# Kernel optimization log

Measured on AMD Instinct MI355X. Metric: run time of the kernel, lower is better.

## Reference

```python
import jax, jax.numpy as jnp
import numpy as np

NUM_NODES = 100000
NUM_EDGES = 625000
IN_FEATURES = 128
OUT_FEATURES = 128


def setup_inputs() -> dict:
    key = jax.random.key(0)
    k1, k2, k3, k4 = jax.random.split(key, 4)
    x = jax.random.normal(k1, (NUM_NODES, IN_FEATURES), dtype=jnp.float32)
    edge_index = jax.random.randint(k2, (2, NUM_EDGES), 0, NUM_NODES, dtype=jnp.int64)
    # Xavier uniform for W (fan_in=IN, fan_out=OUT); B initialized to zeros in the
    # original, but we use small random values so gradients flow through both paths.
    limit = float(np.sqrt(6.0 / (IN_FEATURES + OUT_FEATURES)))
    W = jax.random.uniform(k3, (OUT_FEATURES, IN_FEATURES), dtype=jnp.float32,
                           minval=-limit, maxval=limit)
    B = jax.random.uniform(k4, (OUT_FEATURES, IN_FEATURES), dtype=jnp.float32,
                           minval=-limit, maxval=limit)
    return {"x": x, "edge_index": edge_index, "W": W, "B": B}


def reference(x, edge_index, W, B):
    sources, destinations = edge_index[0], edge_index[1]
    # message: gather destination features, scatter-add into source slots
    messages = x[destinations]                                        # [E, F_in]
    agg = jax.ops.segment_sum(messages, sources, num_segments=x.shape[0])  # [N, F_in]
    # in-degree (w.r.t. sources) normalization; zero-degree -> divide by 1
    deg = jax.ops.segment_sum(jnp.ones((sources.shape[0],), dtype=x.dtype),
                              sources, num_segments=x.shape[0])       # [N]
    deg = jnp.where(deg == 0, jnp.ones_like(deg), deg)
    agg = agg / deg[:, None]
    # update: (W @ messages.T + B @ x.T).T == messages @ W.T + x @ B.T
    out = agg @ W.T + x @ B.T                                         # [N, F_out]
    return out
```

## Files before the change

kernel.cpp:

```cpp
#include <hip/hip_runtime.h>

#define F_IN   128
#define F_OUT  128

typedef __attribute__((ext_vector_type(8))) short short8;
typedef __attribute__((ext_vector_type(4))) float floatx4;

__device__ __forceinline__ float bf16u_to_f_lo(unsigned int u) {
    union { unsigned int i; float f; } c; c.i = u << 16; return c.f;
}
__device__ __forceinline__ float bf16u_to_f_hi(unsigned int u) {
    union { unsigned int i; float f; } c; c.i = u & 0xffff0000u; return c.f;
}
__device__ __forceinline__ unsigned short f_to_bf16(float f) {
    union { float f; unsigned int i; } c; c.f = f;
    unsigned int u = c.i;
    u += 0x7fffu + ((u >> 16) & 1u);
    return (unsigned short)(u >> 16);
}
__device__ __forceinline__ unsigned int pack2(unsigned short a, unsigned short b) {
    return (unsigned int)a | ((unsigned int)b << 16);
}

__global__ void zero_kernel(int* __restrict__ p, long n) {
    long i = (long)blockIdx.x * blockDim.x + threadIdx.x;
    long stride = (long)gridDim.x * blockDim.x;
    for (; i < n; i += stride) p[i] = 0;
}

__global__ void hist_kernel(const int* __restrict__ src, int* __restrict__ cnt, int E) {
    int e = blockIdx.x * blockDim.x + threadIdx.x;
    if (e < E) atomicAdd(&cnt[src[e]], 1);
}

__global__ __launch_bounds__(256) void chunk_sums_kernel(const int* __restrict__ cnt,
                                                         int* __restrict__ partials, int n) {
    __shared__ int s[256];
    int b = blockIdx.x, t = threadIdx.x;
    int base = b * 1024 + t * 4;
    int sum = 0;
#pragma unroll
    for (int j = 0; j < 4; ++j) {
        int i = base + j;
        if (i < n) sum += cnt[i];
    }
    s[t] = sum;
    __syncthreads();
    for (int d = 128; d > 0; d >>= 1) {
        if (t < d) s[t] += s[t + d];
        __syncthreads();
    }
    if (t == 0) partials[b] = s[0];
}

__global__ __launch_bounds__(128) void scan_partials_kernel(const int* __restrict__ partials,
                                                            int* __restrict__ chunk_off, int nch) {
    __shared__ int s[128];
    int t = threadIdx.x;
    s[t] = (t < nch) ? partials[t] : 0;
    __syncthreads();
    for (int d = 1; d < 128; d <<= 1) {
        int val = s[t];
        int add = (t >= d) ? s[t - d] : 0;
        __syncthreads();
        s[t] = val + add;
        __syncthreads();
    }
    if (t < nch) chunk_off[t] = (t > 0) ? s[t - 1] : 0;
}

__global__ __launch_bounds__(256) void scan_chunks_kernel(int* __restrict__ off,
                                                          const int* __restrict__ chunk_off,
                                                          int n) {
    __shared__ int s[256];
    int b = blockIdx.x, t = threadIdx.x;
    int base = b * 1024 + t * 4;
    int v[4];
#pragma unroll
    for (int j = 0; j < 4; ++j) {
        int i = base + j;
        v[j] = (i < n) ? off[i] : 0;
    }
    int l1 = v[0], l2 = l1 + v[1], l3 = l2 + v[2], tot = l3 + v[3];
    s[t] = tot;
    __syncthreads();
    for (int d = 1; d < 256; d <<= 1) {
        int val = s[t];
        int add = (t >= d) ? s[t - d] : 0;
        __syncthreads();
        s[t] = val + add;
        __syncthreads();
    }
    int thr_excl = ((t > 0) ? s[t - 1] : 0) + chunk_off[b];
    if (base + 0 < n) off[base + 0] = thr_excl;
    if (base + 1 < n) off[base + 1] = thr_excl + l1;
    if (base + 2 < n) off[base + 2] = thr_excl + l2;
    if (base + 3 < n) off[base + 3] = thr_excl + l3;
}

__global__ void fill_kernel(const int* __restrict__ ei, int* __restrict__ off,
                            int* __restrict__ dst_sorted, int E) {
    int e = blockIdx.x * blockDim.x + threadIdx.x;
    if (e < E) {
        int s = ei[e];
        int d = ei[E + e];
        int p = atomicAdd(&off[s], 1);
        dst_sorted[p] = d;
    }
}

__global__ __launch_bounds__(256) void convert_x_kernel(const float* __restrict__ x,
                                                        char* __restrict__ outb, int N) {
    long tid = (long)blockIdx.x * blockDim.x + threadIdx.x;
    if (tid >= (long)N * 32) return;
    int row = (int)(tid >> 5);
    int seg = (int)(tid & 31);
    float4 v = *(const float4*)(x + (size_t)row * 128 + seg * 4);
    unsigned short r[4] = {f_to_bf16(v.x), f_to_bf16(v.y), f_to_bf16(v.z), f_to_bf16(v.w)};
    *(ushort4*)(outb + (size_t)row * 512 + 256 + seg * 8) =
        make_ushort4(r[0], r[1], r[2], r[3]);
}

__global__ __launch_bounds__(256) void gather_bf16_kernel(const int* __restrict__ off,
                                                          const int* __restrict__ dst_sorted,
                                                          char* __restrict__ outb, int N) {
    int node = blockIdx.x * 16 + (threadIdx.x >> 4);
    int lane = threadIdx.x & 15;
    if (node >= N) return;
    int start = (node == 0) ? 0 : off[node - 1];
    int end = off[node];
    float acc[8];
#pragma unroll
    for (int i = 0; i < 8; ++i) acc[i] = 0.0f;

    const char* xb = outb;
    int j = start;
    for (; j + 4 <= end; j += 4) {
        int d0 = dst_sorted[j];
        int d1 = dst_sorted[j + 1];
        int d2 = dst_sorted[j + 2];
        int d3 = dst_sorted[j + 3];
        uint4 a = *(const uint4*)(xb + (size_t)d0 * 512 + 256 + lane * 16);
        uint4 b = *(const uint4*)(xb + (size_t)d1 * 512 + 256 + lane * 16);
        uint4 c = *(const uint4*)(xb + (size_t)d2 * 512 + 256 + lane * 16);
        uint4 d = *(const uint4*)(xb + (size_t)d3 * 512 + 256 + lane * 16);
        acc[0] += bf16u_to_f_lo(a.x); acc[1] += bf16u_to_f_hi(a.x);
        acc[2] += bf16u_to_f_lo(a.y); acc[3] += bf16u_to_f_hi(a.y);
        acc[4] += bf16u_to_f_lo(a.z); acc[5] += bf16u_to_f_hi(a.z);
        acc[6] += bf16u_to_f_lo(a.w); acc[7] += bf16u_to_f_hi(a.w);
        acc[0] += bf16u_to_f_lo(b.x); acc[1] += bf16u_to_f_hi(b.x);
        acc[2] += bf16u_to_f_lo(b.y); acc[3] += bf16u_to_f_hi(b.y);
        acc[4] += bf16u_to_f_lo(b.z); acc[5] += bf16u_to_f_hi(b.z);
        acc[6] += bf16u_to_f_lo(b.w); acc[7] += bf16u_to_f_hi(b.w);
        acc[0] += bf16u_to_f_lo(c.x); acc[1] += bf16u_to_f_hi(c.x);
        acc[2] += bf16u_to_f_lo(c.y); acc[3] += bf16u_to_f_hi(c.y);
        acc[4] += bf16u_to_f_lo(c.z); acc[5] += bf16u_to_f_hi(c.z);
        acc[6] += bf16u_to_f_lo(c.w); acc[7] += bf16u_to_f_hi(c.w);
        acc[0] += bf16u_to_f_lo(d.x); acc[1] += bf16u_to_f_hi(d.x);
        acc[2] += bf16u_to_f_lo(d.y); acc[3] += bf16u_to_f_hi(d.y);
        acc[4] += bf16u_to_f_lo(d.z); acc[5] += bf16u_to_f_hi(d.z);
        acc[6] += bf16u_to_f_lo(d.w); acc[7] += bf16u_to_f_hi(d.w);
    }
    for (; j < end; ++j) {
        int d0 = dst_sorted[j];
        uint4 a = *(const uint4*)(xb + (size_t)d0 * 512 + 256 + lane * 16);
        acc[0] += bf16u_to_f_lo(a.x); acc[1] += bf16u_to_f_hi(a.x);
        acc[2] += bf16u_to_f_lo(a.y); acc[3] += bf16u_to_f_hi(a.y);
        acc[4] += bf16u_to_f_lo(a.z); acc[5] += bf16u_to_f_hi(a.z);
        acc[6] += bf16u_to_f_lo(a.w); acc[7] += bf16u_to_f_hi(a.w);
    }
    int deg = end - start;
    float scale = (deg > 0) ? (1.0f / (float)deg) : 1.0f;
    unsigned short r[8];
#pragma unroll
    for (int i = 0; i < 8; ++i) r[i] = f_to_bf16(acc[i] * scale);
    uint4 pk;
    pk.x = pack2(r[0], r[1]);
    pk.y = pack2(r[2], r[3]);
    pk.z = pack2(r[4], r[5]);
    pk.w = pack2(r[6], r[7]);
    *(uint4*)(outb + (size_t)node * 512 + lane * 16) = pk;
}

__global__ __launch_bounds__(256) void gemm_mfma_kernel(const float* __restrict__ W,
                                                        const float* __restrict__ Bm,
                                                        float* __restrict__ out, int N) {
    __shared__ uint4 Bs[4096];
    int t = threadIdx.x;
    int lane = t & 63;
    int w = t >> 6;
    int m16 = lane & 15;
    int quad = lane >> 4;

#pragma unroll
    for (int nt2 = 0; nt2 < 2; ++nt2) {
        int nt = w * 2 + nt2;
        int n = nt * 16 + m16;
#pragma unroll
        for (int s = 0; s < 8; ++s) {
            int kbase = s * 32 + quad * 8;
            const float* srcp = (kbase < 128) ? (W + n * 128 + kbase)
                                              : (Bm + n * 128 + (kbase - 128));
            float4 v0 = *(const float4*)srcp;
            float4 v1 = *(const float4*)(srcp + 4);
            uint4 pk;
            pk.x = pack2(f_to_bf16(v0.x), f_to_bf16(v0.y));
            pk.y = pack2(f_to_bf16(v0.z), f_to_bf16(v0.w));
            pk.z = pack2(f_to_bf16(v1.x), f_to_bf16(v1.y));
            pk.w = pack2(f_to_bf16(v1.z), f_to_bf16(v1.w));
            Bs[(nt * 8 + s) * 64 + lane] = pk;
        }
    }
    __syncthreads();

    int rowbase = blockIdx.x * 128 + w * 32;
    short8 afrag[2][8];
#pragma unroll
    for (int g = 0; g < 2; ++g) {
        int arow = rowbase + g * 16 + m16;
        if (arow > N - 1) arow = N - 1;
        const char* ab = (const char*)out + (size_t)arow * 512;
#pragma unroll
        for (int s = 0; s < 8; ++s)
            afrag[g][s] = *(const short8*)(ab + s * 64 + quad * 16);
    }

    floatx4 acc[2][8];
#pragma unroll
    for (int g = 0; g < 2; ++g)
#pragma unroll
        for (int nt = 0; nt < 8; ++nt) acc[g][nt] = (floatx4){0.f, 0.f, 0.f, 0.f};

#pragma unroll
    for (int nt = 0; nt < 8; ++nt) {
#pragma unroll
        for (int s = 0; s < 8; ++s) {
            short8 bfrag = *(const short8*)&Bs[(nt * 8 + s) * 64 + lane];
            acc[0][nt] = __builtin_amdgcn_mfma_f32_16x16x32_bf16(afrag[0][s], bfrag, acc[0][nt], 0, 0, 0);
            acc[1][nt] = __builtin_amdgcn_mfma_f32_16x16x32_bf16(afrag[1][s], bfrag, acc[1][nt], 0, 0, 0);
        }
    }

#pragma unroll
    for (int g = 0; g < 2; ++g)
#pragma unroll
        for (int nt = 0; nt < 8; ++nt)
#pragma unroll
            for (int r = 0; r < 4; ++r) {
                int gr = rowbase + g * 16 + quad * 4 + r;
                if (gr < N) out[(size_t)gr * 128 + nt * 16 + m16] = acc[g][nt][r];
            }
}

__global__ void invdeg_kernel(int* __restrict__ deg_io, int N) {
    int i = blockIdx.x * blockDim.x + threadIdx.x;
    if (i < N) {
        int d = deg_io[i];
        float inv = (d > 0) ? (1.0f / (float)d) : 1.0f;
        ((float*)deg_io)[i] = inv;
    }
}

__global__ __launch_bounds__(128) void scatter_atomic_kernel(const float* __restrict__ x,
                                                             const int* __restrict__ ei,
                                                             const float* __restrict__ invdeg,
                                                             float* __restrict__ out, int E) {
    int e = blockIdx.x;
    int f = threadIdx.x;
    int s = ei[e];
    int d = ei[E + e];
    float v = x[(long)d * F_IN + f] * invdeg[s];
    atomicAdd(&out[(long)s * F_IN + f], v);
}

__global__ __launch_bounds__(256) void gemm_fused_kernel(const float* __restrict__ x,
                                                         const float* __restrict__ W,
                                                         const float* __restrict__ Bm,
                                                         float* __restrict__ out, int N) {
    __shared__ float As[64][68];
    __shared__ float Ms[64][132];
    int t = threadIdx.x;
    int row0 = blockIdx.x * 64;
    int c0 = (t & 31) * 4;
    int r0 = (t >> 5) * 8;
    float acc[8][4];
#pragma unroll
    for (int i = 0; i < 8; ++i)
#pragma unroll
        for (int j = 0; j < 4; ++j) acc[i][j] = 0.0f;

    for (int kc = 0; kc < 4; ++kc) {
        const float* Asrc = (kc < 2) ? out : x;
        const float* Msrc = (kc < 2) ? W : Bm;
        int k0 = (kc & 1) * 64;
#pragma unroll
        for (int i = 0; i < 4; ++i) {
            int flat = t + 256 * i;
            int m = flat >> 4, ks = flat & 15;
            int row = row0 + m;
            float4 v = make_float4(0.f, 0.f, 0.f, 0.f);
            if (row < N) v = *(const float4*)&Asrc[(long)row * 128 + k0 + ks * 4];
            As[ks * 4 + 0][m] = v.x;
            As[ks * 4 + 1][m] = v.y;
            As[ks * 4 + 2][m] = v.z;
            As[ks * 4 + 3][m] = v.w;
        }
#pragma unroll
        for (int i = 0; i < 8; ++i) {
            int flat = t + 256 * i;
            int c = flat >> 4, ks = flat & 15;
            float4 v = *(const float4*)&Msrc[(long)c * 128 + k0 + ks * 4];
            Ms[ks * 4 + 0][c] = v.x;
            Ms[ks * 4 + 1][c] = v.y;
            Ms[ks * 4 + 2][c] = v.z;
            Ms[ks * 4 + 3][c] = v.w;
        }
        __syncthreads();
#pragma unroll 8
        for (int kk = 0; kk < 64; ++kk) {
            float4 a0 = *(const float4*)&As[kk][r0];
            float4 a1 = *(const float4*)&As[kk][r0 + 4];
            float4 m0 = *(const float4*)&Ms[kk][c0];
            float a[8] = {a0.x, a0.y, a0.z, a0.w, a1.x, a1.y, a1.z, a1.w};
            float m[4] = {m0.x, m0.y, m0.z, m0.w};
#pragma unroll
            for (int i = 0; i < 8; ++i)
#pragma unroll
                for (int j = 0; j < 4; ++j) acc[i][j] += a[i] * m[j];
        }
        __syncthreads();
    }
#pragma unroll
    for (int i = 0; i < 8; ++i) {
        int row = row0 + r0 + i;
        if (row < N) {
            float4 v = make_float4(acc[i][0], acc[i][1], acc[i][2], acc[i][3]);
            *(float4*)&out[(long)row * 128 + c0] = v;
        }
    }
}


extern "C" void kernel_launch(void* const* d_in, const int* in_sizes, int n_in,
                              void* d_out, int out_size, void* d_ws, size_t ws_size,
                              hipStream_t stream) {
    const float* x = (const float*)d_in[0];
    const int* ei = (const int*)d_in[1];
    const float* W = (const float*)d_in[2];
    const float* Bm = (const float*)d_in[3];
    float* out = (float*)d_out;

    const int N = in_sizes[0] / F_IN;
    const int E = in_sizes[1] / 2;
    const int NCHUNK = (N + 1023) / 1024;

    int* off        = (int*)d_ws;
    int* partials   = off + N;
    int* chunk_off  = partials + 128;
    int* dst_sorted = chunk_off + 128;

    const size_t need_csr = ((size_t)N + 256 + (size_t)E) * sizeof(int);
    const size_t need_deg = (size_t)N * sizeof(int);

    if (ws_size >= need_csr) {
        zero_kernel<<<256, 256, 0, stream>>>(off, N);
        hist_kernel<<<(E + 255) / 256, 256, 0, stream>>>(ei, off, E);
        chunk_sums_kernel<<<NCHUNK, 256, 0, stream>>>(off, partials, N);
        scan_partials_kernel<<<1, 128, 0, stream>>>(partials, chunk_off, NCHUNK);
        scan_chunks_kernel<<<NCHUNK, 256, 0, stream>>>(off, chunk_off, N);
        fill_kernel<<<(E + 255) / 256, 256, 0, stream>>>(ei, off, dst_sorted, E);
        {
            long tot = (long)N * 32;
            convert_x_kernel<<<(int)((tot + 255) / 256), 256, 0, stream>>>(x, (char*)out, N);
        }
        gather_bf16_kernel<<<(N + 15) / 16, 256, 0, stream>>>(off, dst_sorted, (char*)out, N);
        gemm_mfma_kernel<<<(N + 127) / 128, 256, 0, stream>>>(W, Bm, out, N);
    } else if (ws_size >= need_deg) {
        int* deg = (int*)d_ws;
        zero_kernel<<<256, 256, 0, stream>>>(deg, N);
        hist_kernel<<<(E + 255) / 256, 256, 0, stream>>>(ei, deg, E);
        invdeg_kernel<<<(N + 255) / 256, 256, 0, stream>>>(deg, N);
        zero_kernel<<<512, 256, 0, stream>>>((int*)out, (long)N * F_IN);
        scatter_atomic_kernel<<<E, 128, 0, stream>>>(x, ei, (const float*)deg, out, E);
        gemm_fused_kernel<<<(N + 63) / 64, 256, 0, stream>>>(x, W, Bm, out, N);
    }
}
```

Baseline: 232.7 us.

## Fold partial-scan into chunk scan and pre-stage bf16 weight fragments

Removes the single-block scan_partials launch by having each scan_chunks block reduce the partial sums of earlier chunks itself. Converts W and B to bf16 MFMA fragment layout once, in an extra block of the x-conversion kernel, and stores them in workspace. The GEMM blocks then copy the prepared fragments straight into LDS with global_load_lds instead of each block re-reading and converting the fp32 weights. This trades one fewer launch and less per-block conversion work for extra workspace and a redundant small reduction in every scan block.

```diff
diff --git a/kernel.cpp b/kernel.cpp
--- a/kernel.cpp
+++ b/kernel.cpp
@@ -20,6 +20,12 @@
 }
 __device__ __forceinline__ unsigned int pack2(unsigned short a, unsigned short b) {
     return (unsigned int)a | ((unsigned int)b << 16);
+}
+
+__device__ __forceinline__ void gload_lds16(const void* g, void* l) {
+    __builtin_amdgcn_global_load_lds(
+        (const __attribute__((address_space(1))) unsigned int*)g,
+        (__attribute__((address_space(3))) unsigned int*)l, 16, 0, 0);
 }
 
 __global__ void zero_kernel(int* __restrict__ p, long n) {
@@ -53,27 +59,13 @@
     if (t == 0) partials[b] = s[0];
 }
 
-__global__ __launch_bounds__(128) void scan_partials_kernel(const int* __restrict__ partials,
-                                                            int* __restrict__ chunk_off, int nch) {
-    __shared__ int s[128];
-    int t = threadIdx.x;
-    s[t] = (t < nch) ? partials[t] : 0;
-    __syncthreads();
-    for (int d = 1; d < 128; d <<= 1) {
-        int val = s[t];
-        int add = (t >= d) ? s[t - d] : 0;
-        __syncthreads();
-        s[t] = val + add;
-        __syncthreads();
-    }
-    if (t < nch) chunk_off[t] = (t > 0) ? s[t - 1] : 0;
-}
-
 __global__ __launch_bounds__(256) void scan_chunks_kernel(int* __restrict__ off,
-                                                          const int* __restrict__ chunk_off,
-                                                          int n) {
+                                                          const int* __restrict__ partials,
+                                                          int n, int nch) {
     __shared__ int s[256];
+    __shared__ int ps[128];
     int b = blockIdx.x, t = threadIdx.x;
+    if (t < 128) ps[t] = (t < nch && t < b) ? partials[t] : 0;
     int base = b * 1024 + t * 4;
     int v[4];
 #pragma unroll
@@ -84,6 +76,10 @@
     int l1 = v[0], l2 = l1 + v[1], l3 = l2 + v[2], tot = l3 + v[3];
     s[t] = tot;
     __syncthreads();
+    for (int d = 64; d > 0; d >>= 1) {
+        if (t < d) ps[t] += ps[t + d];
+        __syncthreads();
+    }
     for (int d = 1; d < 256; d <<= 1) {
         int val = s[t];
         int add = (t >= d) ? s[t - d] : 0;
@@ -91,7 +87,7 @@
         s[t] = val + add;
         __syncthreads();
     }
-    int thr_excl = ((t > 0) ? s[t - 1] : 0) + chunk_off[b];
+    int thr_excl = ((t > 0) ? s[t - 1] : 0) + ps[0];
     if (base + 0 < n) off[base + 0] = thr_excl;
     if (base + 1 < n) off[base + 1] = thr_excl + l1;
     if (base + 2 < n) off[base + 2] = thr_excl + l2;
@@ -110,7 +106,33 @@
 }
 
 __global__ __launch_bounds__(256) void convert_x_kernel(const float* __restrict__ x,
-                                                        char* __restrict__ outb, int N) {
+                                                        char* __restrict__ outb,
+                                                        const float* __restrict__ W,
+                                                        const float* __restrict__ Bm,
+                                                        uint4* __restrict__ bfrag, int N) {
+    if (bfrag && blockIdx.x == gridDim.x - 1) {
+        int t = threadIdx.x;
+#pragma unroll
+        for (int i = 0; i < 16; ++i) {
+            int flat = i * 256 + t;
+            int lane = flat & 63;
+            int idx = flat >> 6;
+            int nt = idx >> 3, sfrag = idx & 7;
+            int n = nt * 16 + (lane & 15);
+            int kbase = sfrag * 32 + (lane >> 4) * 8;
+            const float* srcp = (kbase < 128) ? (W + n * 128 + kbase)
+                                              : (Bm + n * 128 + (kbase - 128));
+            float4 v0 = *(const float4*)srcp;
+            float4 v1 = *(const float4*)(srcp + 4);
+            uint4 pk;
+            pk.x = pack2(f_to_bf16(v0.x), f_to_bf16(v0.y));
+            pk.y = pack2(f_to_bf16(v0.z), f_to_bf16(v0.w));
+            pk.z = pack2(f_to_bf16(v1.x), f_to_bf16(v1.y));
+            pk.w = pack2(f_to_bf16(v1.z), f_to_bf16(v1.w));
+            bfrag[flat] = pk;
+        }
+        return;
+    }
     long tid = (long)blockIdx.x * blockDim.x + threadIdx.x;
     if (tid >= (long)N * 32) return;
     int row = (int)(tid >> 5);
@@ -184,6 +206,7 @@
 
 __global__ __launch_bounds__(256) void gemm_mfma_kernel(const float* __restrict__ W,
                                                         const float* __restrict__ Bm,
+                                                        const uint4* __restrict__ bfrag,
                                                         float* __restrict__ out, int N) {
     __shared__ uint4 Bs[4096];
     int t = threadIdx.x;
@@ -192,23 +215,29 @@
     int m16 = lane & 15;
     int quad = lane >> 4;
 
-#pragma unroll
-    for (int nt2 = 0; nt2 < 2; ++nt2) {
-        int nt = w * 2 + nt2;
-        int n = nt * 16 + m16;
-#pragma unroll
-        for (int s = 0; s < 8; ++s) {
-            int kbase = s * 32 + quad * 8;
-            const float* srcp = (kbase < 128) ? (W + n * 128 + kbase)
-                                              : (Bm + n * 128 + (kbase - 128));
-            float4 v0 = *(const float4*)srcp;
-            float4 v1 = *(const float4*)(srcp + 4);
-            uint4 pk;
-            pk.x = pack2(f_to_bf16(v0.x), f_to_bf16(v0.y));
-            pk.y = pack2(f_to_bf16(v0.z), f_to_bf16(v0.w));
-            pk.z = pack2(f_to_bf16(v1.x), f_to_bf16(v1.y));
-            pk.w = pack2(f_to_bf16(v1.z), f_to_bf16(v1.w));
-            Bs[(nt * 8 + s) * 64 + lane] = pk;
+    if (bfrag) {
+#pragma unroll
+        for (int j = 0; j < 16; ++j)
+            gload_lds16(bfrag + (w * 16 + j) * 64 + lane, &Bs[(w * 16 + j) * 64]);
+    } else {
+#pragma unroll
+        for (int nt2 = 0; nt2 < 2; ++nt2) {
+            int nt = w * 2 + nt2;
+            int n = nt * 16 + m16;
+#pragma unroll
+            for (int s = 0; s < 8; ++s) {
+                int kbase = s * 32 + quad * 8;
+                const float* srcp = (kbase < 128) ? (W + n * 128 + kbase)
+                                                  : (Bm + n * 128 + (kbase - 128));
+                float4 v0 = *(const float4*)srcp;
+                float4 v1 = *(const float4*)(srcp + 4);
+                uint4 pk;
+                pk.x = pack2(f_to_bf16(v0.x), f_to_bf16(v0.y));
+                pk.y = pack2(f_to_bf16(v0.z), f_to_bf16(v0.w));
+                pk.z = pack2(f_to_bf16(v1.x), f_to_bf16(v1.y));
+                pk.w = pack2(f_to_bf16(v1.z), f_to_bf16(v1.w));
+                Bs[(nt * 8 + s) * 64 + lane] = pk;
+            }
         }
     }
     __syncthreads();
@@ -235,9 +264,9 @@
     for (int nt = 0; nt < 8; ++nt) {
 #pragma unroll
         for (int s = 0; s < 8; ++s) {
-            short8 bfrag = *(const short8*)&Bs[(nt * 8 + s) * 64 + lane];
-            acc[0][nt] = __builtin_amdgcn_mfma_f32_16x16x32_bf16(afrag[0][s], bfrag, acc[0][nt], 0, 0, 0);
-            acc[1][nt] = __builtin_amdgcn_mfma_f32_16x16x32_bf16(afrag[1][s], bfrag, acc[1][nt], 0, 0, 0);
+            short8 bf = *(const short8*)&Bs[(nt * 8 + s) * 64 + lane];
+            acc[0][nt] = __builtin_amdgcn_mfma_f32_16x16x32_bf16(afrag[0][s], bf, acc[0][nt], 0, 0, 0);
+            acc[1][nt] = __builtin_amdgcn_mfma_f32_16x16x32_bf16(afrag[1][s], bf, acc[1][nt], 0, 0, 0);
         }
     }
 
@@ -354,27 +383,36 @@
     const int E = in_sizes[1] / 2;
     const int NCHUNK = (N + 1023) / 1024;
 
-    int* off        = (int*)d_ws;
-    int* partials   = off + N;
-    int* chunk_off  = partials + 128;
-    int* dst_sorted = chunk_off + 128;
-
-    const size_t need_csr = ((size_t)N + 256 + (size_t)E) * sizeof(int);
-    const size_t need_deg = (size_t)N * sizeof(int);
+    const size_t need_csr    = ((size_t)N + 128 + (size_t)E) * sizeof(int);
+    const size_t need_staged = need_csr + 4096 * sizeof(uint4);
+    const size_t need_deg    = (size_t)N * sizeof(int);
 
     if (ws_size >= need_csr) {
+        bool staged = (ws_size >= need_staged);
+        uint4* bfrag;
+        int* off;
+        if (staged) {
+            bfrag = (uint4*)d_ws;
+            off   = (int*)(bfrag + 4096);
+        } else {
+            bfrag = nullptr;
+            off   = (int*)d_ws;
+        }
+        int* partials   = off + N;
+        int* dst_sorted = partials + 128;
+
         zero_kernel<<<256, 256, 0, stream>>>(off, N);
         hist_kernel<<<(E + 255) / 256, 256, 0, stream>>>(ei, off, E);
         chunk_sums_kernel<<<NCHUNK, 256, 0, stream>>>(off, partials, N);
-        scan_partials_kernel<<<1, 128, 0, stream>>>(partials, chunk_off, NCHUNK);
-        scan_chunks_kernel<<<NCHUNK, 256, 0, stream>>>(off, chunk_off, N);
+        scan_chunks_kernel<<<NCHUNK, 256, 0, stream>>>(off, partials, N, NCHUNK);
         fill_kernel<<<(E + 255) / 256, 256, 0, stream>>>(ei, off, dst_sorted, E);
         {
             long tot = (long)N * 32;
-            convert_x_kernel<<<(int)((tot + 255) / 256), 256, 0, stream>>>(x, (char*)out, N);
+            int nb = (int)((tot + 255) / 256) + (staged ? 1 : 0);
+            convert_x_kernel<<<nb, 256, 0, stream>>>(x, (char*)out, W, Bm, bfrag, N);
         }
         gather_bf16_kernel<<<(N + 15) / 16, 256, 0, stream>>>(off, dst_sorted, (char*)out, N);
-        gemm_mfma_kernel<<<(N + 127) / 128, 256, 0, stream>>>(W, Bm, out, N);
+        gemm_mfma_kernel<<<(N + 127) / 128, 256, 0, stream>>>(W, Bm, bfrag, out, N);
     } else if (ws_size >= need_deg) {
         int* deg = (int*)d_ws;
         zero_kernel<<<256, 256, 0, stream>>>(deg, N);
```

Result: faster. 222.3 us (-4.5%).
